# Performance work log

Hardware: AMD Instinct MI355X
Metric: run time of the kernel (lower is better)

Reference implementation:

```python
import math
import jax, jax.numpy as jnp
import numpy as np

DEGREE = 5
LN_EPS = 1e-5


def hermite_psi(C, r):
    # x_d = tanh(linspace(-1,1,C)) * (sqrt(2r+1)+1), shape [C]
    x_d = jnp.tanh(jnp.linspace(-1.0, 1.0, C)) * (math.sqrt(2 * r + 1) + 1.0)
    g = jnp.exp(-x_d ** 2 / 2.0)
    rows = [math.pi ** (-0.25) * g]
    if r > 0:
        rows.append(math.sqrt(2.0) * math.pi ** (-0.25) * x_d * g)
    for k in range(2, r + 1):
        rows.append(math.sqrt(2.0 / k) * x_d * rows[-1] - math.sqrt((k - 1) / k) * rows[-2])
    return jnp.stack(rows)  # [r+1, C]


def setup_inputs() -> dict:
    key = jax.random.key(0)
    k1, k2 = jax.random.split(key)
    B, C, H, W = 16, 512, 64, 64
    O = 512
    x = jax.random.normal(k1, (B, C, H, W), dtype=jnp.float32)
    ln_w = jnp.ones((C,), dtype=jnp.float32)
    ln_b = jnp.zeros((C,), dtype=jnp.float32)
    fc_w = jax.random.normal(k2, (O, C), dtype=jnp.float32) * (1.0 / math.sqrt(C))
    fc_b = jnp.zeros((O,), dtype=jnp.float32)
    return {"x": x, "ln_w": ln_w, "ln_b": ln_b, "fc_w": fc_w, "fc_b": fc_b}


def reference(x, ln_w, ln_b, fc_w, fc_b):
    B, C, H, W = x.shape
    O = fc_w.shape[0]
    # [B, HW, C]
    q = x.reshape(B, C, H * W).transpose(0, 2, 1)
    # LayerNorm over channels (biased variance, eps=1e-5)
    mu = q.mean(axis=-1, keepdims=True)
    var = ((q - mu) ** 2).mean(axis=-1, keepdims=True)
    q = (q - mu) / jnp.sqrt(var + LN_EPS) * ln_w + ln_b
    # Constant Hermite basis [r+1, C]
    psi = hermite_psi(C, DEGREE).astype(x.dtype)
    # Tiny cross-attention: scores [B, HW, r+1]
    scores = jnp.einsum('bnc,rc->bnr', q, psi) / math.sqrt(C)
    attn = jax.nn.softmax(scores, axis=-1)
    y = jnp.einsum('bnr,rc->bnc', attn, psi)  # [B, HW, C]
    # 1x1 conv == pointwise GEMM over channels
    out = jnp.einsum('bnc,oc->bon', y, fc_w) + fc_b[None, :, None]
    return out.reshape(B, O, H, W)
```

## Files before the change

kernel.cpp:

```cpp
#include <hip/hip_runtime.h>
#include <math.h>

#define C 512
#define NPIX 4096
#define BATCH 16
#define O 512
#define R 6
#define LN_EPS 1e-5f


__global__ __launch_bounds__(512) void setup_psi(const float* __restrict__ lnw,
                                                 const float* __restrict__ lnb,
                                                 float* __restrict__ ws) {
    __shared__ float sh_psi[R * C];
    const int c = threadIdx.x;
    float t = -1.0f + 2.0f * (float)c / 511.0f;
    float xd = tanhf(t) * 4.31662479035539984911f;
    float g = expf(-0.5f * xd * xd);
    const float pi_m14 = 0.75112554446494248286f;
    float rows[R];
    rows[0] = pi_m14 * g;
    rows[1] = 1.41421356237309504880f * pi_m14 * xd * g;
    #pragma unroll
    for (int k = 2; k <= 5; ++k)
        rows[k] = sqrtf(2.0f / k) * xd * rows[k - 1] - sqrtf((k - 1.0f) / k) * rows[k - 2];
    float w = lnw[c];
    #pragma unroll
    for (int r = 0; r < R; ++r) {
        sh_psi[r * C + c] = rows[r];
        ws[8192 + r * C + c] = rows[r];
        ws[c * 8 + r] = rows[r] * w;
    }
    __syncthreads();
    const int wv = threadIdx.x >> 6;
    const int l = threadIdx.x & 63;
    #pragma unroll
    for (int pass = 0; pass < 2; ++pass) {
        int combo = pass * 8 + wv;
        if (combo < 12) {
            int r = (combo < 6) ? combo : combo - 6;
            const float* vec = (combo < 6) ? lnw : lnb;
            float acc = 0.f;
            #pragma unroll
            for (int j = 0; j < 8; ++j) {
                int cc = l + 64 * j;
                acc += vec[cc] * sh_psi[r * C + cc];
            }
            #pragma unroll
            for (int m = 32; m >= 1; m >>= 1) acc += __shfl_xor(acc, m, 64);
            if (l == 0) ws[(combo < 6 ? 4096 : 4104) + r] = acc;
        }
    }
}

__global__ __launch_bounds__(64) void setup_M(const float* __restrict__ fcw,
                                              const float* __restrict__ fcb,
                                              float* __restrict__ ws) {
    const int o = blockIdx.x;
    const int lane = threadIdx.x;
    const float* psi = ws + 8192;
    float acc[R] = {0.f, 0.f, 0.f, 0.f, 0.f, 0.f};
    for (int c = lane; c < C; c += 64) {
        float w = fcw[o * C + c];
        #pragma unroll
        for (int r = 0; r < R; ++r) acc[r] += psi[r * C + c] * w;
    }
    #pragma unroll
    for (int r = 0; r < R; ++r)
        for (int m = 32; m >= 1; m >>= 1) acc[r] += __shfl_xor(acc[r], m, 64);
    if (lane == 0) {
        float bias = fcb[o];
        #pragma unroll
        for (int r = 0; r < R; ++r) ws[4112 + r * O + o] = acc[r] + bias;
    }
}

__global__ __launch_bounds__(256, 4) void fused_main(const float* __restrict__ x,
                                                     const float* __restrict__ ws,
                                                     float* __restrict__ out) {
    __shared__ float shW[C * 8];
    __shared__ float shM[R * O];
    __shared__ float part[4][8][64];
    __shared__ float attnS[R][64];

    const int tid = threadIdx.x;
    const int wv = tid >> 6;
    const int l = tid & 63;
    const int b = blockIdx.x >> 6;
    const int ng = blockIdx.x & 63;
    const int n0 = ng << 6;

    {
        const float4* wsrc = (const float4*)ws;
        float4* wdst = (float4*)shW;
        for (int i = tid; i < 1024; i += 256) wdst[i] = wsrc[i];
        const float4* msrc = (const float4*)(ws + 4112);
        float4* mdst = (float4*)shM;
        for (int i = tid; i < 768; i += 256) mdst[i] = msrc[i];
    }
    __syncthreads();

    const float* xb = x + ((size_t)(b * C + (wv << 7)) << 12) + n0 + l;
    float s = 0.f, ss = 0.f;
    float a0 = 0.f, a1 = 0.f, a2 = 0.f, a3 = 0.f, a4 = 0.f, a5 = 0.f;
    #pragma unroll 16
    for (int i = 0; i < 128; ++i) {
        float xv = xb[(size_t)i << 12];
        const float* wr = &shW[((wv << 7) + i) << 3];
        float4 w03 = *(const float4*)wr;
        float2 w45 = *(const float2*)(wr + 4);
        s += xv;
        ss += xv * xv;
        a0 += xv * w03.x;
        a1 += xv * w03.y;
        a2 += xv * w03.z;
        a3 += xv * w03.w;
        a4 += xv * w45.x;
        a5 += xv * w45.y;
    }
    part[wv][0][l] = s;  part[wv][1][l] = ss;
    part[wv][2][l] = a0; part[wv][3][l] = a1;
    part[wv][4][l] = a2; part[wv][5][l] = a3;
    part[wv][6][l] = a4; part[wv][7][l] = a5;
    __syncthreads();

    if (tid < 64) {
        float v[8];
        #pragma unroll
        for (int j = 0; j < 8; ++j)
            v[j] = part[0][j][tid] + part[1][j][tid] + part[2][j][tid] + part[3][j][tid];
        float mu = v[0] * (1.0f / 512.0f);
        float var = v[1] * (1.0f / 512.0f) - mu * mu;
        float rsig = rsqrtf(var + LN_EPS);
        const float invsq = 0.04419417382415922f;
        float sc[R], mx = -1e30f;
        #pragma unroll
        for (int r = 0; r < R; ++r) {
            float swp = ws[4096 + r], sbp = ws[4104 + r];
            sc[r] = ((v[2 + r] - mu * swp) * rsig + sbp) * invsq;
            mx = fmaxf(mx, sc[r]);
        }
        float es = 0.f, at[R];
        #pragma unroll
        for (int r = 0; r < R; ++r) { at[r] = expf(sc[r] - mx); es += at[r]; }
        float inv = 1.0f / es;
        #pragma unroll
        for (int r = 0; r < R; ++r) attnS[r][tid] = at[r] * inv;
    }
    __syncthreads();

    const int pxg = (tid & 15) << 2;
    const int og = tid >> 4;
    float4 a4v[R];
    #pragma unroll
    for (int r = 0; r < R; ++r) a4v[r] = *(const float4*)&attnS[r][pxg];
    float* ob = out + ((size_t)(b * O) << 12) + n0 + pxg;
    #pragma unroll 8
    for (int k = 0; k < 32; ++k) {
        int o = og + (k << 4);
        float m0 = shM[0 * O + o], m1 = shM[1 * O + o], m2 = shM[2 * O + o];
        float m3 = shM[3 * O + o], m4 = shM[4 * O + o], m5 = shM[5 * O + o];
        float4 res;
        res.x = a4v[0].x * m0 + a4v[1].x * m1 + a4v[2].x * m2 + a4v[3].x * m3 + a4v[4].x * m4 + a4v[5].x * m5;
        res.y = a4v[0].y * m0 + a4v[1].y * m1 + a4v[2].y * m2 + a4v[3].y * m3 + a4v[4].y * m4 + a4v[5].y * m5;
        res.z = a4v[0].z * m0 + a4v[1].z * m1 + a4v[2].z * m2 + a4v[3].z * m3 + a4v[4].z * m4 + a4v[5].z * m5;
        res.w = a4v[0].w * m0 + a4v[1].w * m1 + a4v[2].w * m2 + a4v[3].w * m3 + a4v[4].w * m4 + a4v[5].w * m5;
        *(float4*)(ob + ((size_t)o << 12)) = res;
    }
}

extern "C" void kernel_launch(void* const* d_in, const int* in_sizes, int n_in,
                              void* d_out, int out_size, void* d_ws, size_t ws_size,
                              hipStream_t stream) {
    const float* x    = (const float*)d_in[0];
    const float* ln_w = (const float*)d_in[1];
    const float* ln_b = (const float*)d_in[2];
    const float* fc_w = (const float*)d_in[3];
    const float* fc_b = (const float*)d_in[4];
    float* out = (float*)d_out;
    float* ws = (float*)d_ws;

    setup_psi<<<1, 512, 0, stream>>>(ln_w, ln_b, ws);
    setup_M<<<O, 64, 0, stream>>>(fc_w, fc_b, ws);
    fused_main<<<BATCH * 64, 256, 0, stream>>>(x, ws, out);
}
```

Baseline: 272.3 us.

## Split fused kernel into stats/attention and broadcast-GEMM kernels with nontemporal stores

The single fused kernel is replaced by two kernels. A stats kernel reads x with float4 loads, with 256 pixels per block and 8 waves splitting channels, and writes the softmax attention weights to workspace. A separate broadcast kernel with many more blocks expands the attention weights times M into the 128MB output using nontemporal stores. The split is meant to raise parallelism and write bandwidth for the output-dominated phase. In exchange it adds a launch and an attention round-trip through global memory, and the stats kernel now has only 256 blocks.

Measured after the change: 245.4 us. 9.9% less time.

```diff
diff --git a/kernel.cpp b/kernel.cpp
--- a/kernel.cpp
+++ b/kernel.cpp
@@ -7,6 +7,9 @@
 #define O 512
 #define R 6
 #define LN_EPS 1e-5f
+#define ATTN_OFF 16384
+
+typedef float vf4 __attribute__((ext_vector_type(4)));
 
 
 __global__ __launch_bounds__(512) void setup_psi(const float* __restrict__ lnw,
@@ -75,60 +78,57 @@
     }
 }
 
-__global__ __launch_bounds__(256, 4) void fused_main(const float* __restrict__ x,
-                                                     const float* __restrict__ ws,
-                                                     float* __restrict__ out) {
-    __shared__ float shW[C * 8];
-    __shared__ float shM[R * O];
-    __shared__ float part[4][8][64];
-    __shared__ float attnS[R][64];
-
+__global__ __launch_bounds__(512) void stats_kernel(const float* __restrict__ x,
+                                                    const float* __restrict__ ws,
+                                                    float* __restrict__ attn) {
+    __shared__ float part[8][8][256];
     const int tid = threadIdx.x;
     const int wv = tid >> 6;
     const int l = tid & 63;
-    const int b = blockIdx.x >> 6;
-    const int ng = blockIdx.x & 63;
-    const int n0 = ng << 6;
-
-    {
-        const float4* wsrc = (const float4*)ws;
-        float4* wdst = (float4*)shW;
-        for (int i = tid; i < 1024; i += 256) wdst[i] = wsrc[i];
-        const float4* msrc = (const float4*)(ws + 4112);
-        float4* mdst = (float4*)shM;
-        for (int i = tid; i < 768; i += 256) mdst[i] = msrc[i];
-    }
+    const int b = blockIdx.x >> 4;
+    const int pxg = blockIdx.x & 15;
+    const int n0 = pxg << 8;
+    const int wuni = __builtin_amdgcn_readfirstlane(wv);
+
+    const float* xb = x + (((size_t)(b * C + (wuni << 6))) << 12) + n0 + (l << 2);
+    const float* wbase = ws + ((size_t)(wuni << 6) << 3);
+
+    float4 s = {0.f,0.f,0.f,0.f}, ss = s;
+    float4 a0 = s, a1 = s, a2 = s, a3 = s, a4 = s, a5 = s;
+    #pragma unroll 8
+    for (int i = 0; i < 64; ++i) {
+        float4 xv = *(const float4*)(xb + ((size_t)i << 12));
+        const float* wr = wbase + (i << 3);
+        float w0 = wr[0], w1 = wr[1], w2 = wr[2];
+        float w3 = wr[3], w4 = wr[4], w5 = wr[5];
+        s.x += xv.x;  s.y += xv.y;  s.z += xv.z;  s.w += xv.w;
+        ss.x += xv.x * xv.x; ss.y += xv.y * xv.y; ss.z += xv.z * xv.z; ss.w += xv.w * xv.w;
+        a0.x += xv.x * w0; a0.y += xv.y * w0; a0.z += xv.z * w0; a0.w += xv.w * w0;
+        a1.x += xv.x * w1; a1.y += xv.y * w1; a1.z += xv.z * w1; a1.w += xv.w * w1;
+        a2.x += xv.x * w2; a2.y += xv.y * w2; a2.z += xv.z * w2; a2.w += xv.w * w2;
+        a3.x += xv.x * w3; a3.y += xv.y * w3; a3.z += xv.z * w3; a3.w += xv.w * w3;
+        a4.x += xv.x * w4; a4.y += xv.y * w4; a4.z += xv.z * w4; a4.w += xv.w * w4;
+        a5.x += xv.x * w5; a5.y += xv.y * w5; a5.z += xv.z * w5; a5.w += xv.w * w5;
+    }
+    *(float4*)&part[wv][0][l << 2] = s;
+    *(float4*)&part[wv][1][l << 2] = ss;
+    *(float4*)&part[wv][2][l << 2] = a0;
+    *(float4*)&part[wv][3][l << 2] = a1;
+    *(float4*)&part[wv][4][l << 2] = a2;
+    *(float4*)&part[wv][5][l << 2] = a3;
+    *(float4*)&part[wv][6][l << 2] = a4;
+    *(float4*)&part[wv][7][l << 2] = a5;
     __syncthreads();
 
-    const float* xb = x + ((size_t)(b * C + (wv << 7)) << 12) + n0 + l;
-    float s = 0.f, ss = 0.f;
-    float a0 = 0.f, a1 = 0.f, a2 = 0.f, a3 = 0.f, a4 = 0.f, a5 = 0.f;
-    #pragma unroll 16
-    for (int i = 0; i < 128; ++i) {
-        float xv = xb[(size_t)i << 12];
-        const float* wr = &shW[((wv << 7) + i) << 3];
-        float4 w03 = *(const float4*)wr;
-        float2 w45 = *(const float2*)(wr + 4);
-        s += xv;
-        ss += xv * xv;
-        a0 += xv * w03.x;
-        a1 += xv * w03.y;
-        a2 += xv * w03.z;
-        a3 += xv * w03.w;
-        a4 += xv * w45.x;
-        a5 += xv * w45.y;
-    }
-    part[wv][0][l] = s;  part[wv][1][l] = ss;
-    part[wv][2][l] = a0; part[wv][3][l] = a1;
-    part[wv][4][l] = a2; part[wv][5][l] = a3;
-    part[wv][6][l] = a4; part[wv][7][l] = a5;
-    __syncthreads();
-
-    if (tid < 64) {
+    if (tid < 256) {
         float v[8];
         #pragma unroll
-        for (int j = 0; j < 8; ++j)
-            v[j] = part[0][j][tid] + part[1][j][tid] + part[2][j][tid] + part[3][j][tid];
+        for (int st = 0; st < 8; ++st) {
+            float acc = 0.f;
+            #pragma unroll
+            for (int w = 0; w < 8; ++w) acc += part[w][st][tid];
+            v[st] = acc;
+        }
         float mu = v[0] * (1.0f / 512.0f);
         float var = v[1] * (1.0f / 512.0f) - mu * mu;
         float rsig = rsqrtf(var + LN_EPS);
@@ -145,27 +145,42 @@
         for (int r = 0; r < R; ++r) { at[r] = expf(sc[r] - mx); es += at[r]; }
         float inv = 1.0f / es;
         #pragma unroll
-        for (int r = 0; r < R; ++r) attnS[r][tid] = at[r] * inv;
-    }
-    __syncthreads();
-
-    const int pxg = (tid & 15) << 2;
-    const int og = tid >> 4;
-    float4 a4v[R];
-    #pragma unroll
-    for (int r = 0; r < R; ++r) a4v[r] = *(const float4*)&attnS[r][pxg];
-    float* ob = out + ((size_t)(b * O) << 12) + n0 + pxg;
-    #pragma unroll 8
-    for (int k = 0; k < 32; ++k) {
-        int o = og + (k << 4);
-        float m0 = shM[0 * O + o], m1 = shM[1 * O + o], m2 = shM[2 * O + o];
-        float m3 = shM[3 * O + o], m4 = shM[4 * O + o], m5 = shM[5 * O + o];
-        float4 res;
-        res.x = a4v[0].x * m0 + a4v[1].x * m1 + a4v[2].x * m2 + a4v[3].x * m3 + a4v[4].x * m4 + a4v[5].x * m5;
-        res.y = a4v[0].y * m0 + a4v[1].y * m1 + a4v[2].y * m2 + a4v[3].y * m3 + a4v[4].y * m4 + a4v[5].y * m5;
-        res.z = a4v[0].z * m0 + a4v[1].z * m1 + a4v[2].z * m2 + a4v[3].z * m3 + a4v[4].z * m4 + a4v[5].z * m5;
-        res.w = a4v[0].w * m0 + a4v[1].w * m1 + a4v[2].w * m2 + a4v[3].w * m3 + a4v[4].w * m4 + a4v[5].w * m5;
-        *(float4*)(ob + ((size_t)o << 12)) = res;
+        for (int r = 0; r < R; ++r)
+            attn[(((size_t)(b * 6 + r)) << 12) + n0 + tid] = at[r] * inv;
+    }
+}
+
+__global__ __launch_bounds__(256) void bcast_kernel(const float* __restrict__ ws,
+                                                    float* __restrict__ out) {
+    const int tid = threadIdx.x;
+    const int bid = blockIdx.x;
+    const int b = bid >> 8;
+    const int pxg = (bid >> 6) & 3;
+    const int og = bid & 63;
+    const int n = (pxg << 10) + (tid << 2);
+
+    const float* attn = ws + ATTN_OFF;
+    float4 ar[R];
+    #pragma unroll
+    for (int r = 0; r < R; ++r)
+        ar[r] = *(const float4*)(attn + (((size_t)(b * 6 + r)) << 12) + n);
+
+    float* ob = out + (((size_t)(b * O + (og << 3))) << 12) + n;
+    #pragma unroll
+    for (int j = 0; j < 8; ++j) {
+        int o = (og << 3) + j;
+        float m0 = ws[4112 + 0 * O + o];
+        float m1 = ws[4112 + 1 * O + o];
+        float m2 = ws[4112 + 2 * O + o];
+        float m3 = ws[4112 + 3 * O + o];
+        float m4 = ws[4112 + 4 * O + o];
+        float m5 = ws[4112 + 5 * O + o];
+        vf4 res;
+        res.x = ar[0].x * m0 + ar[1].x * m1 + ar[2].x * m2 + ar[3].x * m3 + ar[4].x * m4 + ar[5].x * m5;
+        res.y = ar[0].y * m0 + ar[1].y * m1 + ar[2].y * m2 + ar[3].y * m3 + ar[4].y * m4 + ar[5].y * m5;
+        res.z = ar[0].z * m0 + ar[1].z * m1 + ar[2].z * m2 + ar[3].z * m3 + ar[4].z * m4 + ar[5].z * m5;
+        res.w = ar[0].w * m0 + ar[1].w * m1 + ar[2].w * m2 + ar[3].w * m3 + ar[4].w * m4 + ar[5].w * m5;
+        __builtin_nontemporal_store(res, (vf4*)(ob + ((size_t)j << 12)));
     }
 }
 
@@ -182,5 +197,6 @@
 
     setup_psi<<<1, 512, 0, stream>>>(ln_w, ln_b, ws);
     setup_M<<<O, 64, 0, stream>>>(fc_w, fc_b, ws);
-    fused_main<<<BATCH * 64, 256, 0, stream>>>(x, ws, out);
-}
+    stats_kernel<<<BATCH * 16, 512, 0, stream>>>(x, ws, ws + ATTN_OFF);
+    bcast_kernel<<<4096, 256, 0, stream>>>(ws, out);
+}
```
